# Kernel tuning notes

Measured on AMD Instinct MI355X. Metric: run time of the kernel, lower is better.

The kernel has to match this reference:

```python
import jax, jax.numpy as jnp
import numpy as np

N = 100000
E = 1600000
IN_CH = 128
OUT_CH = 128
NUM_REL = 16
NUM_BASES = 8


def setup_inputs() -> dict:
    key = jax.random.key(0)
    k1, k2, k3, k4, k5, k6 = jax.random.split(key, 6)
    x = jax.random.normal(k1, (N, IN_CH), dtype=jnp.float32)
    edge_index = jax.random.randint(k2, (2, E), 0, N, dtype=jnp.int64)
    edge_type = jax.random.randint(k3, (E,), 0, NUM_REL, dtype=jnp.int64)
    # glorot-style init for basis weights (last slot = root weight) and comp
    wscale = np.sqrt(6.0 / (IN_CH + OUT_CH)).astype(np.float32)
    weight = jax.random.uniform(k4, (NUM_BASES + 1, IN_CH, OUT_CH), dtype=jnp.float32,
                                minval=-wscale, maxval=wscale)
    cscale = np.sqrt(6.0 / (NUM_REL + NUM_BASES)).astype(np.float32)
    comp = jax.random.uniform(k5, (NUM_REL, NUM_BASES), dtype=jnp.float32,
                              minval=-cscale, maxval=cscale)
    bias = jnp.zeros((OUT_CH,), dtype=jnp.float32)
    return {"x": x, "weight": weight, "comp": comp, "bias": bias,
            "edge_index": edge_index, "edge_type": edge_type, "num_nodes": N}


def reference(x, weight, comp, bias, edge_index, edge_type, num_nodes):
    """RGCN with basis decomposition, mean aggregation, root weight + bias.

    agg[i, b, :] = (1/deg(i)) * sum_{e: dst(e)=i} comp[etype(e), b] * x[src(e)]
    out = concat_b(agg, x_root) @ weight.reshape(-1, out_ch) + bias
    """
    src = edge_index[0]
    dst = edge_index[1]
    num_bases = comp.shape[1]
    coeff = comp[edge_type]            # [E, B] per-edge basis coefficients
    msg = x[src]                       # [E, in] gathered neighbor features
    # per-basis scatter-add into destination nodes (loop over small fixed B)
    aggs = [jax.ops.segment_sum(msg * coeff[:, b:b + 1], dst, num_segments=num_nodes)
            for b in range(num_bases)]
    agg = jnp.stack(aggs, axis=1)      # [N, B, in]
    # mean normalization by in-degree of destination node
    deg = jax.ops.segment_sum(jnp.ones((src.shape[0],), dtype=x.dtype), dst,
                              num_segments=num_nodes)
    agg = agg / jnp.maximum(deg, 1.0)[:, None, None]
    # [N, (B+1)*in]: bases first, then root features (matches weight layout)
    feat = jnp.concatenate([agg.reshape(num_nodes, -1), x], axis=1)
    out = feat @ weight.reshape(-1, weight.shape[-1]) + bias
    return out
```

## Files before the change

kernel.cpp:

```cpp
#include <hip/hip_runtime.h>
#include <hip/hip_bf16.h>
#include <stdint.h>


#define FPAD 1160
#define SCAT_CH 8192
#define PADV 16
#define BKCAP 2560
#define CSTRIDE 3584

typedef __attribute__((ext_vector_type(8))) __bf16 bf16x8;
typedef __attribute__((ext_vector_type(4))) float f32x4;
typedef __attribute__((ext_vector_type(2))) float f32x2;

#define RFL(v) __builtin_amdgcn_readfirstlane(v)

__global__ __launch_bounds__(256) void k_ps(const float* __restrict__ x,
                                            uint8_t* __restrict__ xq,
                                            __hip_bfloat16* __restrict__ xb, int n4,
                                            const float* __restrict__ W,
                                            __hip_bfloat16* __restrict__ Wf,
                                            const float* __restrict__ comp,
                                            float* __restrict__ comp17,
                                            const int* __restrict__ src,
                                            const int* __restrict__ dst,
                                            const int* __restrict__ et,
                                            int E, int NB,
                                            int* __restrict__ cursor,
                                            int* __restrict__ brec,
                                            int scB, int xbB, int wpB) {
    extern __shared__ int sm[];
    int b = blockIdx.x;
    if (b < scB) {
        int* cnt = sm;
        int* gb  = sm + NB;
        for (int i = threadIdx.x; i < NB; i += 256) cnt[i] = 0;
        __syncthreads();
        int e0 = b * SCAT_CH;
        int e1 = min(e0 + SCAT_CH, E);
        for (int e = e0 + threadIdx.x; e < e1; e += 256)
            atomicAdd(&cnt[dst[e] >> 7], 1);
        __syncthreads();
        for (int i = threadIdx.x; i < NB; i += 256) {
            int c = cnt[i];
            gb[i] = c ? atomicAdd(&cursor[i], c) : 0;
        }
        __syncthreads();
        for (int i = threadIdx.x; i < NB; i += 256) cnt[i] = 0;
        __syncthreads();
        for (int e = e0 + threadIdx.x; e < e1; e += 256) {
            int d = dst[e];
            int bk = d >> 7;
            int off = gb[bk] + atomicAdd(&cnt[bk], 1);
            if (off < BKCAP)
                brec[bk * BKCAP + off] = (src[e] << 11) | ((d & 127) << 4) | (et[e] & 15);
        }
    } else if (b < scB + xbB) {
        int i = (b - scB) * 256 + threadIdx.x;
        if (i < n4) {
            float4 v = ((const float4*)x)[i];
            uint32_t q = __builtin_amdgcn_cvt_pk_fp8_f32(v.x, v.y, 0u, 0);
            q = __builtin_amdgcn_cvt_pk_fp8_f32(v.z, v.w, q, 1);
            ((uint32_t*)xq)[i] = q;
            __hip_bfloat16 h0 = __float2bfloat16(v.x), h1 = __float2bfloat16(v.y);
            __hip_bfloat16 h2 = __float2bfloat16(v.z), h3 = __float2bfloat16(v.w);
            uint32_t p0 = ((uint32_t)*(uint16_t*)&h1 << 16) | *(uint16_t*)&h0;
            uint32_t p1 = ((uint32_t)*(uint16_t*)&h3 << 16) | *(uint16_t*)&h2;
            ((uint2*)xb)[i] = make_uint2(p0, p1);
        }
    } else if (b < scB + xbB + wpB) {
        int idx = (b - scB - xbB) * 256 + threadIdx.x;
        if (idx < 1152 * 128) {
            int k = idx >> 7, n = idx & 127;
            int kb = k >> 5, hi = (k >> 3) & 3, j = k & 7;
            Wf[((((kb << 2) + hi) << 7 | n) << 3) | j] = __float2bfloat16(W[idx]);
        }
    } else {
        int t = threadIdx.x;
        if (t < 136) comp17[t] = (t < 128) ? comp[t] : 0.f;
    }
}

__global__ __launch_bounds__(256) void k_bsort(const int* __restrict__ brec,
                                               const int* __restrict__ cursor,
                                               int N,
                                               int* __restrict__ rps,
                                               int* __restrict__ dga,
                                               int* __restrict__ csr) {
    __shared__ int cnt[128], st[128];
    int b = blockIdx.x;
    int ne = min(cursor[b], BKCAP);
    int rbase = b * BKCAP;
    int pbase = b * CSTRIDE;
    int t = threadIdx.x;
    if (t < 128) cnt[t] = 0;
    __syncthreads();
    for (int i = t; i < ne; i += 256)
        atomicAdd(&cnt[(brec[rbase + i] >> 4) & 127], 1);
    __syncthreads();
    if (t < 128) st[t] = (cnt[t] + 7) & ~7;
    __syncthreads();
    for (int off = 1; off < 128; off <<= 1) {
        int u = 0;
        if (t < 128 && t >= off) u = st[t - off];
        __syncthreads();
        if (t < 128) st[t] += u;
        __syncthreads();
    }
    if (t < 128) {
        int c = cnt[t];
        int pc = (c + 7) & ~7;
        int pexcl = st[t] - pc;
        int d = b * 128 + t;
        if (d < N) { rps[d] = pbase + pexcl; dga[d] = c; }
        for (int k = c; k < pc; k++) csr[pbase + pexcl + k] = PADV;
        cnt[t] = pexcl;
    } else if (t >= 128 && t < 152) {
        int idx = st[127] + (t - 128);
        if (idx < CSTRIDE) csr[pbase + idx] = PADV;
    }
    __syncthreads();
    for (int i = t; i < ne; i += 256) {
        int r = brec[rbase + i];
        int d7 = (r >> 4) & 127;
        int off = atomicAdd(&cnt[d7], 1);
        csr[pbase + off] = ((r >> 11) << 5) | (r & 15);
    }
}

#define GATH(pp) ((uint32_t)xq16[(uint32_t)((pp) >> 5) * 64u + (uint32_t)lane])

#define CONS1(pp, raw) do {                                               \
    uint32_t _r = (raw);                                                  \
    float _x0 = __builtin_amdgcn_cvt_f32_fp8(_r, 0);                      \
    float _x1 = __builtin_amdgcn_cvt_f32_fp8(_r, 1);                      \
    const f32x2* _cf = (const f32x2*)(comp17 + ((pp) & 31) * 8);          \
    f32x2 _xx0 = (f32x2){_x0, _x0};                                       \
    f32x2 _xx1 = (f32x2){_x1, _x1};                                       \
    f32x2 _c0 = _cf[0], _c1 = _cf[1], _c2 = _cf[2], _c3 = _cf[3];         \
    a0[0] += _c0 * _xx0; a0[1] += _c1 * _xx0;                             \
    a0[2] += _c2 * _xx0; a0[3] += _c3 * _xx0;                             \
    a1[0] += _c0 * _xx1; a1[1] += _c1 * _xx1;                             \
    a1[2] += _c2 * _xx1; a1[3] += _c3 * _xx1;                             \
} while (0)

__global__ __launch_bounds__(512, 8) void k_fused(const uint8_t* __restrict__ xq,
                                                  const __hip_bfloat16* __restrict__ xb,
                                                  const float* __restrict__ comp17,
                                                  const int* __restrict__ rps,
                                                  const int* __restrict__ dga,
                                                  const int* __restrict__ csr,
                                                  const __hip_bfloat16* __restrict__ Wf,
                                                  const float* __restrict__ bias,
                                                  float* __restrict__ out, int M) {
    __shared__ __hip_bfloat16 fl[16][FPAD];
    __shared__ int snext;
    const uint16_t* __restrict__ xq16 = (const uint16_t*)xq;
    const uint32_t* __restrict__ xb32 = (const uint32_t*)xb;
    int t = threadIdx.x;
    int wid = t >> 6, lane = t & 63;
    int i0 = blockIdx.x * 16;
    if (t == 0) snext = 0;
    __syncthreads();

    #pragma unroll 1
    while (true) {
        int grab = 0;
        if (lane == 0) grab = atomicAdd(&snext, 1);
        int lr = RFL(__shfl(grab, 0));
        if (lr >= 16) break;
        int iu = i0 + lr;
        f32x2 a0[4], a1[4];
        #pragma unroll
        for (int b = 0; b < 4; b++) { a0[b] = (f32x2){0.f, 0.f}; a1[b] = (f32x2){0.f, 0.f}; }
        int s0 = 0, dg = 0;
        if (iu < M) {
            s0 = RFL(rps[iu]);
            dg = RFL(dga[iu]);
        }

        if (dg > 0) {
            int plen = (dg + 7) & ~7;
            int s1 = s0 + plen;
            int jj = s0;
            int p0 = RFL(csr[jj]),     p1 = RFL(csr[jj + 1]);
            int p2 = RFL(csr[jj + 2]), p3 = RFL(csr[jj + 3]);
            int p4 = RFL(csr[jj + 4]), p5 = RFL(csr[jj + 5]);
            int p6 = RFL(csr[jj + 6]), p7 = RFL(csr[jj + 7]);
            uint32_t w0 = GATH(p0), w1 = GATH(p1), w2 = GATH(p2), w3 = GATH(p3);
            uint32_t w4 = GATH(p4), w5 = GATH(p5), w6 = GATH(p6), w7 = GATH(p7);
            int q0 = RFL(csr[jj + 8]),  q1 = RFL(csr[jj + 9]);
            int q2 = RFL(csr[jj + 10]), q3 = RFL(csr[jj + 11]);
            int q4 = RFL(csr[jj + 12]), q5 = RFL(csr[jj + 13]);
            int q6 = RFL(csr[jj + 14]), q7 = RFL(csr[jj + 15]);
            uint32_t v0 = GATH(q0), v1 = GATH(q1), v2 = GATH(q2), v3 = GATH(q3);
            uint32_t v4 = GATH(q4), v5 = GATH(q5), v6 = GATH(q6), v7 = GATH(q7);

            #pragma unroll 1
            while (jj + 16 < s1) {
                int r0 = RFL(csr[jj + 16]), r1 = RFL(csr[jj + 17]);
                int r2 = RFL(csr[jj + 18]), r3 = RFL(csr[jj + 19]);
                int r4 = RFL(csr[jj + 20]), r5 = RFL(csr[jj + 21]);
                int r6 = RFL(csr[jj + 22]), r7 = RFL(csr[jj + 23]);
                uint32_t u0 = GATH(r0), u1 = GATH(r1), u2 = GATH(r2), u3 = GATH(r3);
                uint32_t u4 = GATH(r4), u5 = GATH(r5), u6 = GATH(r6), u7 = GATH(r7);
                CONS1(p0, w0); CONS1(p1, w1); CONS1(p2, w2); CONS1(p3, w3);
                CONS1(p4, w4); CONS1(p5, w5); CONS1(p6, w6); CONS1(p7, w7);
                p0 = q0; p1 = q1; p2 = q2; p3 = q3;
                p4 = q4; p5 = q5; p6 = q6; p7 = q7;
                w0 = v0; w1 = v1; w2 = v2; w3 = v3;
                w4 = v4; w5 = v5; w6 = v6; w7 = v7;
                q0 = r0; q1 = r1; q2 = r2; q3 = r3;
                q4 = r4; q5 = r5; q6 = r6; q7 = r7;
                v0 = u0; v1 = u1; v2 = u2; v3 = u3;
                v4 = u4; v5 = u5; v6 = u6; v7 = u7;
                jj += 8;
            }
            CONS1(p0, w0); CONS1(p1, w1); CONS1(p2, w2); CONS1(p3, w3);
            CONS1(p4, w4); CONS1(p5, w5); CONS1(p6, w6); CONS1(p7, w7);
            if (jj + 8 < s1) {
                CONS1(q0, v0); CONS1(q1, v1); CONS1(q2, v2); CONS1(q3, v3);
                CONS1(q4, v4); CONS1(q5, v5); CONS1(q6, v6); CONS1(q7, v7);
            }
        }

        float inv = 1.0f / fmaxf((float)dg, 1.0f);
        #pragma unroll
        for (int b = 0; b < 8; b++) {
            __hip_bfloat16 h0 = __float2bfloat16(a0[b >> 1][b & 1] * inv);
            __hip_bfloat16 h1 = __float2bfloat16(a1[b >> 1][b & 1] * inv);
            uint32_t pk = ((uint32_t)*(uint16_t*)&h1 << 16) | *(uint16_t*)&h0;
            *(uint32_t*)&fl[lr][b * 128 + lane * 2] = pk;
        }
        uint32_t rr = (iu < M) ? xb32[(uint32_t)iu * 64u + lane] : 0u;
        *(uint32_t*)&fl[lr][1024 + lane * 2] = rr;
    }

    int lo = lane & 15, hi = lane >> 4;
    int wcol = wid * 16 + lo;
    const bf16x8* wv = (const bf16x8*)Wf;
    bf16x8 bA = wv[(hi << 7) + wcol];
    bf16x8 bB = wv[(((1 << 2) + hi) << 7) + wcol];
    float bs = bias[wcol];
    __syncthreads();

    f32x4 acc = (f32x4){0.f, 0.f, 0.f, 0.f};
    bf16x8 aA = *(const bf16x8*)&fl[lo][hi * 8];
    bf16x8 aB = *(const bf16x8*)&fl[lo][32 + hi * 8];
    #pragma unroll 4
    for (int kb = 0; kb < 34; kb++) {
        bf16x8 aN = *(const bf16x8*)&fl[lo][(kb + 2) * 32 + hi * 8];
        bf16x8 bN = wv[((((kb + 2) << 2) + hi) << 7) + wcol];
        acc = __builtin_amdgcn_mfma_f32_16x16x32_bf16(aA, bA, acc, 0, 0, 0);
        aA = aB; bA = bB; aB = aN; bB = bN;
    }
    acc = __builtin_amdgcn_mfma_f32_16x16x32_bf16(aA, bA, acc, 0, 0, 0);
    acc = __builtin_amdgcn_mfma_f32_16x16x32_bf16(aB, bB, acc, 0, 0, 0);

    #pragma unroll
    for (int q = 0; q < 4; q++) {
        int row = i0 + hi * 4 + q;
        if (row < M)
            out[(size_t)row * 128 + wcol] = acc[q] + bs;
    }
}

extern "C" void kernel_launch(void* const* d_in, const int* in_sizes, int n_in,
                              void* d_out, int out_size, void* d_ws, size_t ws_size,
                              hipStream_t stream) {
    const float* x      = (const float*)d_in[0];
    const float* weight = (const float*)d_in[1];
    const float* comp   = (const float*)d_in[2];
    const float* bias   = (const float*)d_in[3];
    const int*   eidx   = (const int*)d_in[4];
    const int*   etype  = (const int*)d_in[5];

    int N = in_sizes[0] / 128;
    int E = in_sizes[5];
    const int* srcA = eidx;
    const int* dstA = eidx + E;
    int NB = (N + 127) >> 7;

    uint8_t* ws = (uint8_t*)d_ws;
    size_t off = 0;
    auto take = [&](size_t bytes) -> void* {
        void* p = ws + off;
        off = (off + bytes + 255) & ~(size_t)255;
        return p;
    };
    uint8_t* xq        = (uint8_t*)take((size_t)N * 128);
    __hip_bfloat16* xb = (__hip_bfloat16*)take((size_t)N * 128 * sizeof(__hip_bfloat16));
    __hip_bfloat16* Wf = (__hip_bfloat16*)take((size_t)1152 * 128 * sizeof(__hip_bfloat16));
    float* comp17 = (float*)take(136 * sizeof(float));
    int* rps     = (int*)take((size_t)N * sizeof(int));
    int* dga     = (int*)take((size_t)N * sizeof(int));
    int* cursor  = (int*)take((size_t)NB * sizeof(int));
    int* brec    = (int*)take((size_t)NB * BKCAP * sizeof(int));
    int* csr     = (int*)take((size_t)NB * CSTRIDE * sizeof(int));
    (void)ws_size;

    int n4 = N * 128 / 4;
    int xbB = (n4 + 255) / 256;
    int wpB = (1152 * 128 + 255) / 256;
    int scB = (E + SCAT_CH - 1) / SCAT_CH;

    hipMemsetAsync(cursor, 0, (size_t)NB * sizeof(int), stream);
    k_ps<<<scB + xbB + wpB + 1, 256, 2 * NB * sizeof(int), stream>>>(
        x, xq, xb, n4, weight, Wf, comp, comp17,
        srcA, dstA, etype, E, NB, cursor, brec, scB, xbB, wpB);
    k_bsort<<<NB, 256, 0, stream>>>(brec, cursor, N, rps, dga, csr);
    k_fused<<<(N + 15) / 16, 512, 0, stream>>>(xq, xb, comp17, rps, dga, csr,
                                               Wf, bias, (float*)d_out, N);
}
```

Baseline: 170.0 us.

## Prefetch next row's CSR indices and gathers across row iterations

Software-pipelines the per-wave row loop. The wave grabs its next destination row and issues that row's first CSR index loads and fp8 feature gathers before it drains the current row's tail, so the start-of-row load latency overlaps with compute. The second batch of gathers is issued after the row's outputs are written. This adds live registers under the existing (512, 8) launch bounds, which may cause spills or lower occupancy, and it relies on padded CSR reads being safe when a row has zero degree.

```diff
diff --git a/kernel.cpp b/kernel.cpp
--- a/kernel.cpp
+++ b/kernel.cpp
@@ -144,6 +144,9 @@
     a1[2] += _c2 * _xx1; a1[3] += _c3 * _xx1;                             \
 } while (0)
 
+#define GRAB(lrv) do { int _g = 0; if (lane == 0) _g = atomicAdd(&snext, 1); \
+                       lrv = RFL(__shfl(_g, 0)); } while (0)
+
 __global__ __launch_bounds__(512, 8) void k_fused(const uint8_t* __restrict__ xq,
                                                   const __hip_bfloat16* __restrict__ xb,
                                                   const float* __restrict__ comp17,
@@ -163,59 +166,81 @@
     if (t == 0) snext = 0;
     __syncthreads();
 
+    int lr;
+    GRAB(lr);
+    int iu = 0, s0 = 0, dg = 0;
+    int p0 = PADV, p1 = PADV, p2 = PADV, p3 = PADV;
+    int p4 = PADV, p5 = PADV, p6 = PADV, p7 = PADV;
+    int q0 = PADV, q1 = PADV, q2 = PADV, q3 = PADV;
+    int q4 = PADV, q5 = PADV, q6 = PADV, q7 = PADV;
+    uint32_t w0 = 0, w1 = 0, w2 = 0, w3 = 0, w4 = 0, w5 = 0, w6 = 0, w7 = 0;
+    uint32_t v0 = 0, v1 = 0, v2 = 0, v3 = 0, v4 = 0, v5 = 0, v6 = 0, v7 = 0;
+    if (lr < 16) {
+        iu = i0 + lr;
+        if (iu < M) { s0 = RFL(rps[iu]); dg = RFL(dga[iu]); }
+        p0 = RFL(csr[s0]);     p1 = RFL(csr[s0 + 1]);
+        p2 = RFL(csr[s0 + 2]); p3 = RFL(csr[s0 + 3]);
+        p4 = RFL(csr[s0 + 4]); p5 = RFL(csr[s0 + 5]);
+        p6 = RFL(csr[s0 + 6]); p7 = RFL(csr[s0 + 7]);
+        w0 = GATH(p0); w1 = GATH(p1); w2 = GATH(p2); w3 = GATH(p3);
+        w4 = GATH(p4); w5 = GATH(p5); w6 = GATH(p6); w7 = GATH(p7);
+        q0 = RFL(csr[s0 + 8]);  q1 = RFL(csr[s0 + 9]);
+        q2 = RFL(csr[s0 + 10]), q3 = RFL(csr[s0 + 11]);
+        q4 = RFL(csr[s0 + 12]); q5 = RFL(csr[s0 + 13]);
+        q6 = RFL(csr[s0 + 14]); q7 = RFL(csr[s0 + 15]);
+        v0 = GATH(q0); v1 = GATH(q1); v2 = GATH(q2); v3 = GATH(q3);
+        v4 = GATH(q4); v5 = GATH(q5); v6 = GATH(q6); v7 = GATH(q7);
+    }
+
     #pragma unroll 1
-    while (true) {
-        int grab = 0;
-        if (lane == 0) grab = atomicAdd(&snext, 1);
-        int lr = RFL(__shfl(grab, 0));
-        if (lr >= 16) break;
-        int iu = i0 + lr;
+    while (lr < 16) {
         f32x2 a0[4], a1[4];
         #pragma unroll
         for (int b = 0; b < 4; b++) { a0[b] = (f32x2){0.f, 0.f}; a1[b] = (f32x2){0.f, 0.f}; }
-        int s0 = 0, dg = 0;
-        if (iu < M) {
-            s0 = RFL(rps[iu]);
-            dg = RFL(dga[iu]);
+        int plen = (dg + 7) & ~7;
+        int s1 = s0 + plen;
+        int jj = s0;
+
+        #pragma unroll 1
+        while (jj + 16 < s1) {
+            int r0 = RFL(csr[jj + 16]), r1 = RFL(csr[jj + 17]);
+            int r2 = RFL(csr[jj + 18]), r3 = RFL(csr[jj + 19]);
+            int r4 = RFL(csr[jj + 20]), r5 = RFL(csr[jj + 21]);
+            int r6 = RFL(csr[jj + 22]), r7 = RFL(csr[jj + 23]);
+            uint32_t u0 = GATH(r0), u1 = GATH(r1), u2 = GATH(r2), u3 = GATH(r3);
+            uint32_t u4 = GATH(r4), u5 = GATH(r5), u6 = GATH(r6), u7 = GATH(r7);
+            CONS1(p0, w0); CONS1(p1, w1); CONS1(p2, w2); CONS1(p3, w3);
+            CONS1(p4, w4); CONS1(p5, w5); CONS1(p6, w6); CONS1(p7, w7);
+            p0 = q0; p1 = q1; p2 = q2; p3 = q3;
+            p4 = q4; p5 = q5; p6 = q6; p7 = q7;
+            w0 = v0; w1 = v1; w2 = v2; w3 = v3;
+            w4 = v4; w5 = v5; w6 = v6; w7 = v7;
+            q0 = r0; q1 = r1; q2 = r2; q3 = r3;
+            q4 = r4; q5 = r5; q6 = r6; q7 = r7;
+            v0 = u0; v1 = u1; v2 = u2; v3 = u3;
+            v4 = u4; v5 = u5; v6 = u6; v7 = u7;
+            jj += 8;
+        }
+
+        int lrn;
+        GRAB(lrn);
+        int iun = 0, s0n = 0, dgn = 0;
+        int pn0 = PADV, pn1 = PADV, pn2 = PADV, pn3 = PADV;
+        int pn4 = PADV, pn5 = PADV, pn6 = PADV, pn7 = PADV;
+        uint32_t wn0 = 0, wn1 = 0, wn2 = 0, wn3 = 0;
+        uint32_t wn4 = 0, wn5 = 0, wn6 = 0, wn7 = 0;
+        if (lrn < 16) {
+            iun = i0 + lrn;
+            if (iun < M) { s0n = RFL(rps[iun]); dgn = RFL(dga[iun]); }
+            pn0 = RFL(csr[s0n]);     pn1 = RFL(csr[s0n + 1]);
+            pn2 = RFL(csr[s0n + 2]); pn3 = RFL(csr[s0n + 3]);
+            pn4 = RFL(csr[s0n + 4]); pn5 = RFL(csr[s0n + 5]);
+            pn6 = RFL(csr[s0n + 6]); pn7 = RFL(csr[s0n + 7]);
+            wn0 = GATH(pn0); wn1 = GATH(pn1); wn2 = GATH(pn2); wn3 = GATH(pn3);
+            wn4 = GATH(pn4); wn5 = GATH(pn5); wn6 = GATH(pn6); wn7 = GATH(pn7);
         }
 
         if (dg > 0) {
-            int plen = (dg + 7) & ~7;
-            int s1 = s0 + plen;
-            int jj = s0;
-            int p0 = RFL(csr[jj]),     p1 = RFL(csr[jj + 1]);
-            int p2 = RFL(csr[jj + 2]), p3 = RFL(csr[jj + 3]);
-            int p4 = RFL(csr[jj + 4]), p5 = RFL(csr[jj + 5]);
-            int p6 = RFL(csr[jj + 6]), p7 = RFL(csr[jj + 7]);
-            uint32_t w0 = GATH(p0), w1 = GATH(p1), w2 = GATH(p2), w3 = GATH(p3);
-            uint32_t w4 = GATH(p4), w5 = GATH(p5), w6 = GATH(p6), w7 = GATH(p7);
-            int q0 = RFL(csr[jj + 8]),  q1 = RFL(csr[jj + 9]);
-            int q2 = RFL(csr[jj + 10]), q3 = RFL(csr[jj + 11]);
-            int q4 = RFL(csr[jj + 12]), q5 = RFL(csr[jj + 13]);
-            int q6 = RFL(csr[jj + 14]), q7 = RFL(csr[jj + 15]);
-            uint32_t v0 = GATH(q0), v1 = GATH(q1), v2 = GATH(q2), v3 = GATH(q3);
-            uint32_t v4 = GATH(q4), v5 = GATH(q5), v6 = GATH(q6), v7 = GATH(q7);
-
-            #pragma unroll 1
-            while (jj + 16 < s1) {
-                int r0 = RFL(csr[jj + 16]), r1 = RFL(csr[jj + 17]);
-                int r2 = RFL(csr[jj + 18]), r3 = RFL(csr[jj + 19]);
-                int r4 = RFL(csr[jj + 20]), r5 = RFL(csr[jj + 21]);
-                int r6 = RFL(csr[jj + 22]), r7 = RFL(csr[jj + 23]);
-                uint32_t u0 = GATH(r0), u1 = GATH(r1), u2 = GATH(r2), u3 = GATH(r3);
-                uint32_t u4 = GATH(r4), u5 = GATH(r5), u6 = GATH(r6), u7 = GATH(r7);
-                CONS1(p0, w0); CONS1(p1, w1); CONS1(p2, w2); CONS1(p3, w3);
-                CONS1(p4, w4); CONS1(p5, w5); CONS1(p6, w6); CONS1(p7, w7);
-                p0 = q0; p1 = q1; p2 = q2; p3 = q3;
-                p4 = q4; p5 = q5; p6 = q6; p7 = q7;
-                w0 = v0; w1 = v1; w2 = v2; w3 = v3;
-                w4 = v4; w5 = v5; w6 = v6; w7 = v7;
-                q0 = r0; q1 = r1; q2 = r2; q3 = r3;
-                q4 = r4; q5 = r5; q6 = r6; q7 = r7;
-                v0 = u0; v1 = u1; v2 = u2; v3 = u3;
-                v4 = u4; v5 = u5; v6 = u6; v7 = u7;
-                jj += 8;
-            }
             CONS1(p0, w0); CONS1(p1, w1); CONS1(p2, w2); CONS1(p3, w3);
             CONS1(p4, w4); CONS1(p5, w5); CONS1(p6, w6); CONS1(p7, w7);
             if (jj + 8 < s1) {
@@ -234,6 +259,20 @@
         }
         uint32_t rr = (iu < M) ? xb32[(uint32_t)iu * 64u + lane] : 0u;
         *(uint32_t*)&fl[lr][1024 + lane * 2] = rr;
+
+        lr = lrn; iu = iun; s0 = s0n; dg = dgn;
+        if (lr < 16) {
+            p0 = pn0; p1 = pn1; p2 = pn2; p3 = pn3;
+            p4 = pn4; p5 = pn5; p6 = pn6; p7 = pn7;
+            w0 = wn0; w1 = wn1; w2 = wn2; w3 = wn3;
+            w4 = wn4; w5 = wn5; w6 = wn6; w7 = wn7;
+            q0 = RFL(csr[s0 + 8]);  q1 = RFL(csr[s0 + 9]);
+            q2 = RFL(csr[s0 + 10]); q3 = RFL(csr[s0 + 11]);
+            q4 = RFL(csr[s0 + 12]); q5 = RFL(csr[s0 + 13]);
+            q6 = RFL(csr[s0 + 14]); q7 = RFL(csr[s0 + 15]);
+            v0 = GATH(q0); v1 = GATH(q1); v2 = GATH(q2); v3 = GATH(q3);
+            v4 = GATH(q4); v5 = GATH(q5); v6 = GATH(q6); v7 = GATH(q7);
+        }
     }
 
     int lo = lane & 15, hi = lane >> 4;
```

New measurement: 171.4 us. About the same (+0.8%).
